# Kernel tuning notes

Measured on AMD Instinct MI355X. Metric: run time of the kernel, lower is better.

Reference implementation:

```python
import jax, jax.numpy as jnp
import numpy as np
import math

B, T, C = 4, 2048, 2048
N_HEAD, N_KV = 16, 4
HD = C // N_HEAD          # 128
N_REP = N_HEAD // N_KV    # 4


def setup_inputs() -> dict:
    key = jax.random.key(0)
    ks = jax.random.split(key, 5)
    x = jax.random.normal(ks[0], (B, T, C), dtype=jnp.float32)
    s = 0.02
    wq = jax.random.normal(ks[1], (C, N_HEAD * HD), dtype=jnp.float32) * s
    wk = jax.random.normal(ks[2], (C, N_KV * HD), dtype=jnp.float32) * s
    wv = jax.random.normal(ks[3], (C, N_KV * HD), dtype=jnp.float32) * s
    wo = jax.random.normal(ks[4], (C, C), dtype=jnp.float32) * s
    # RoPE table: cos/sin pairs, equivalent to torch polar freqs_cis (theta=10000)
    inv_freq = 1.0 / (10000.0 ** (jnp.arange(0, HD, 2, dtype=jnp.float32) / HD))  # (HD/2,)
    ang = jnp.arange(T, dtype=jnp.float32)[:, None] * inv_freq[None, :]           # (T, HD/2)
    freqs_cis = jnp.stack([jnp.cos(ang), jnp.sin(ang)], axis=-1)                  # (T, HD/2, 2)
    return {"x": x, "freqs_cis": freqs_cis, "wq": wq, "wk": wk, "wv": wv, "wo": wo}


def _rope(t, freqs_cis):
    # t: (B, T, H, HD); complex multiply on (even, odd) pairs
    tp = t.reshape(*t.shape[:-1], HD // 2, 2)
    a, b = tp[..., 0], tp[..., 1]
    c = freqs_cis[: t.shape[1], :, 0][None, :, None, :]  # (1,T,1,HD/2)
    s = freqs_cis[: t.shape[1], :, 1][None, :, None, :]
    out = jnp.stack([a * c - b * s, a * s + b * c], axis=-1)
    return out.reshape(t.shape).astype(t.dtype)


def reference(x, freqs_cis, wq, wk, wv, wo):
    q = (x @ wq).reshape(B, T, N_HEAD, HD)
    k = (x @ wk).reshape(B, T, N_KV, HD)
    v = (x @ wv).reshape(B, T, N_KV, HD)
    q = _rope(q, freqs_cis)
    k = _rope(k, freqs_cis)
    # GQA attention without materializing repeated K/V: group q heads by kv head
    qg = q.reshape(B, T, N_KV, N_REP, HD)
    scale = 1.0 / math.sqrt(HD)
    att = jnp.einsum('btgrd,bsgd->bgrts', qg, k) * scale   # (B,G,R,T,S)
    causal = jnp.tril(jnp.ones((T, T), dtype=bool))
    att = jnp.where(causal, att, jnp.finfo(att.dtype).min)
    att = jax.nn.softmax(att, axis=-1)
    y = jnp.einsum('bgrts,bsgd->btgrd', att, v).reshape(B, T, C)
    y = y @ wo
    return y
```

## Files before the change

### kernel.cpp

```cpp
#include <hip/hip_runtime.h>
#include <math.h>
#include <stdint.h>

#define B_ 4
#define T_ 2048
#define C_ 2048
#define NH 16
#define NKV 4
#define HD 128
#define NREP 4
#define KVC (NKV*HD)
#define QSTR 3072

typedef __attribute__((ext_vector_type(8))) __bf16 bf16x8;
typedef __attribute__((ext_vector_type(4))) float floatx4;

#define GLOBAL_AS __attribute__((address_space(1)))
#define LDS_AS __attribute__((address_space(3)))

__device__ __forceinline__ void gl2lds16(const unsigned short* g, unsigned short* l) {
  __builtin_amdgcn_global_load_lds((const GLOBAL_AS unsigned int*)g,
                                   (LDS_AS unsigned int*)l, 16, 0, 0);
}

__device__ __forceinline__ float b2f(unsigned short u) {
  union { unsigned int i; float f; } v; v.i = ((unsigned int)u) << 16; return v.f;
}
__device__ __forceinline__ unsigned short f2b(float f) {
  union { float f; unsigned int i; } v; v.f = f;
  unsigned int r = v.i + 0x7fffu + ((v.i >> 16) & 1u);
  return (unsigned short)(r >> 16);
}

__global__ void cvt_bf16_kernel(const float* __restrict__ X,
                                unsigned short* __restrict__ Y, int n) {
  int i = (blockIdx.x * 256 + threadIdx.x) * 4;
  if (i >= n) return;
  float4 v = *(const float4*)(X + i);
  ushort4 o;
  o.x = f2b(v.x); o.y = f2b(v.y); o.z = f2b(v.z); o.w = f2b(v.w);
  *(ushort4*)(Y + i) = o;
}

__global__ void transpose_cvt_kernel(const float* __restrict__ W,
                                     unsigned short* __restrict__ Wt,
                                     int K, int N) {
  __shared__ float tile[32][33];
  int n = blockIdx.x * 32 + threadIdx.x;
  int kbase = blockIdx.y * 32;
  #pragma unroll
  for (int i = 0; i < 32; i += 8)
    tile[threadIdx.y + i][threadIdx.x] = W[(size_t)(kbase + threadIdx.y + i) * N + n];
  __syncthreads();
  int k = kbase + threadIdx.x;
  int nb = blockIdx.x * 32;
  #pragma unroll
  for (int i = 0; i < 32; i += 8)
    Wt[(size_t)(nb + threadIdx.y + i) * K + k] = f2b(tile[threadIdx.x][threadIdx.y + i]);
}

__global__ void transpose_v_kernel(const unsigned short* __restrict__ V,
                                   unsigned short* __restrict__ Vt) {
  __shared__ unsigned short tile[32][33];
  int d0 = blockIdx.x * 32;
  int sg = blockIdx.y * 32;
  int b = sg >> 11;
  int s0 = sg & (T_ - 1);
  #pragma unroll
  for (int i = 0; i < 32; i += 8)
    tile[threadIdx.y + i][threadIdx.x] =
        V[(size_t)(sg + threadIdx.y + i) * QSTR + d0 + threadIdx.x];
  __syncthreads();
  #pragma unroll
  for (int i = 0; i < 32; i += 8) {
    int d = d0 + threadIdx.y + i;
    int g = d >> 7, dl = d & 127;
    Vt[((size_t)(b * NKV + g) * HD + dl) * T_ + s0 + threadIdx.x] =
        tile[threadIdx.x][threadIdx.y + i];
  }
}

template<int STORE_BF16>
__global__ __launch_bounds__(512, 2) void gemm256_bt(
    const unsigned short* __restrict__ A,
    const unsigned short* __restrict__ Bt,
    void* __restrict__ Cout,
    int M, int N, int K)
{
  __shared__ unsigned short Lds[65536];

  int tid = threadIdx.x;

  int nbx = gridDim.x;
  int nwg = nbx * gridDim.y;
  int orig = blockIdx.y * nbx + blockIdx.x;
  int cpx = nwg >> 3;
  int swz = (orig & 7) * cpx + (orig >> 3);
  int m0 = (swz % nbx) * 256;
  int n0 = (swz / nbx) * 256;

  int wave = tid >> 6, lane = tid & 63;
  int fr = lane & 15, kg = lane >> 4;
  int slot = kg ^ ((fr >> 1) & 3);
  int wm_off = (wave >> 2) * 128;
  int wn_off = (wave & 3) * 64;

  int rowoff = wave * 16 + (lane >> 2);
  int kgs = (lane & 3) ^ ((lane >> 3) & 3);
  const unsigned short* Asrc = A  + (size_t)(m0 + rowoff) * K + kgs * 8;
  const unsigned short* Bsrc = Bt + (size_t)(n0 + rowoff) * K + kgs * 8;
  size_t rstep = (size_t)128 * K;

  int abase = (wm_off + fr) * 32 + slot * 8;
  int bbase = 8192 + (wn_off + fr) * 32 + slot * 8;

  floatx4 acc[8][4];
  #pragma unroll
  for (int i = 0; i < 8; i++)
    #pragma unroll
    for (int j = 0; j < 4; j++)
      acc[i][j] = (floatx4){0.f, 0.f, 0.f, 0.f};

  int nt = K >> 6;

  #define STAGE_HALF(tn, kkh, isB) do {                                        \
    const unsigned short* s_ = ((isB) ? Bsrc : Asrc) + (size_t)(tn) * 64 + (kkh) * 32; \
    unsigned short* d_ = &Lds[(((tn) & 1) << 15) + ((kkh) << 14) + ((isB) << 13) + (wave << 9)]; \
    gl2lds16(s_, d_);                                                          \
    gl2lds16(s_ + rstep, d_ + 4096);                                           \
  } while (0)

  STAGE_HALF(0, 0, 0); STAGE_HALF(0, 0, 1); STAGE_HALF(0, 1, 0); STAGE_HALF(0, 1, 1);
  asm volatile("s_waitcnt vmcnt(4)" ::: "memory");
  __builtin_amdgcn_s_barrier();

  bf16x8 bfrag[4];
  for (int t = 0; t < nt; ++t) {
    int cb = (t & 1) << 15;
    int more = (t + 1 < nt);
    #pragma unroll
    for (int p = 0; p < 4; ++p) {
      const int kkc = p >> 1, mhc = p & 1;
      if (mhc == 0) {
        #pragma unroll
        for (int j = 0; j < 4; ++j) {
          union { uint4 u; bf16x8 v; } tb;
          tb.u = *(const uint4*)&Lds[cb + bbase + (kkc << 14) + j * 512];
          bfrag[j] = tb.v;
        }
      }
      bf16x8 af[4];
      #pragma unroll
      for (int i = 0; i < 4; ++i) {
        union { uint4 u; bf16x8 v; } ta;
        ta.u = *(const uint4*)&Lds[cb + abase + (kkc << 14) + (mhc * 4 + i) * 512];
        af[i] = ta.v;
      }
      if (more) STAGE_HALF(t + 1, kkc, mhc);
      if (p == 1) {
        if (more) asm volatile("s_waitcnt vmcnt(4)" ::: "memory");
        else      asm volatile("s_waitcnt vmcnt(0)" ::: "memory");
      } else if (p == 3) {
        if (more) asm volatile("s_waitcnt vmcnt(4)" ::: "memory");
      }
      __builtin_amdgcn_s_barrier();
      asm volatile("s_waitcnt lgkmcnt(0)" ::: "memory");
      __builtin_amdgcn_s_setprio(1);
      #pragma unroll
      for (int i = 0; i < 4; ++i)
        #pragma unroll
        for (int j = 0; j < 4; ++j)
          acc[mhc * 4 + i][j] =
              __builtin_amdgcn_mfma_f32_16x16x32_bf16(af[i], bfrag[j], acc[mhc * 4 + i][j], 0, 0, 0);
      __builtin_amdgcn_s_setprio(0);
      __builtin_amdgcn_s_barrier();
    }
  }
  #undef STAGE_HALF

  int erow = kg * 4;
  #pragma unroll
  for (int i = 0; i < 8; ++i)
    #pragma unroll
    for (int j = 0; j < 4; ++j) {
      int gm = m0 + wm_off + i * 16 + erow;
      int gn = n0 + wn_off + j * 16 + fr;
      #pragma unroll
      for (int r = 0; r < 4; ++r) {
        float v = acc[i][j][r];
        if (STORE_BF16)
          ((unsigned short*)Cout)[(size_t)(gm + r) * N + gn] = f2b(v);
        else
          ((float*)Cout)[(size_t)(gm + r) * N + gn] = v;
      }
    }
}

__global__ void rope_kernel(unsigned short* __restrict__ X,
                            const float* __restrict__ FC, int nheads, int stride) {
  long long idx = (long long)blockIdx.x * 256 + threadIdx.x;
  int p = (int)(idx & (HD / 2 - 1));
  long long t1 = idx >> 6;
  int h = (int)(t1 % nheads);
  long long row = t1 / nheads;
  int t = (int)(row & (T_ - 1));
  float c = FC[((size_t)t * (HD / 2) + p) * 2 + 0];
  float s = FC[((size_t)t * (HD / 2) + p) * 2 + 1];
  unsigned short* ptr = X + row * (size_t)stride + h * HD + 2 * p;
  float a = b2f(ptr[0]), b = b2f(ptr[1]);
  ptr[0] = f2b(a * c - b * s);
  ptr[1] = f2b(a * s + b * c);
}

#define ABR 128
#define ABC 64
#define KLD 136
#define VLD 72
#define PLD 72

__global__ __launch_bounds__(256, 3) void attn_mfma_kernel(
    const unsigned short* __restrict__ Q,
    const unsigned short* __restrict__ Kg,
    const unsigned short* __restrict__ Vt,
    unsigned short* __restrict__ O)
{
  __shared__ unsigned short KPs[128 * PLD];
  __shared__ unsigned short Vs[HD * VLD];

  int bh = blockIdx.x;
  int qt = (int)(gridDim.y - 1 - blockIdx.y);
  int b = bh >> 4, h = bh & 15, g = h >> 2;
  int tid = threadIdx.x, wave = tid >> 6, lane = tid & 63;
  int fr = lane & 15, kg = lane >> 4, erow = 4 * kg;

  bf16x8 qf[2][4];
  #pragma unroll
  for (int rt = 0; rt < 2; rt++) {
    const unsigned short* qrow =
        Q + (size_t)(b * T_ + qt * ABR + wave * 32 + rt * 16 + fr) * QSTR + h * HD;
    #pragma unroll
    for (int kk = 0; kk < 4; kk++) {
      union { uint4 u; bf16x8 v; } t;
      t.u = *(const uint4*)(qrow + kk * 32 + kg * 8);
      qf[rt][kk] = t.v;
    }
  }

  floatx4 oacc[2][8];
  #pragma unroll
  for (int rt = 0; rt < 2; rt++)
    #pragma unroll
    for (int d = 0; d < 8; d++) oacc[rt][d] = (floatx4){0.f, 0.f, 0.f, 0.f};
  float rsum[2][4];
  #pragma unroll
  for (int rt = 0; rt < 2; rt++)
    #pragma unroll
    for (int r = 0; r < 4; r++) rsum[rt][r] = 0.f;

  const float scale = 0.08838834764831845f;
  const float MOFF = 9.0f;

  size_t krow0 = (size_t)(b * T_) * QSTR + g * HD;
  size_t vbase = ((size_t)(b * NKV + g) * HD) * T_;
  int q0 = qt * ABR + wave * 32;
  int nit = 2 * qt + 2;

  int sr = tid >> 2, kc4 = (tid & 3) * 8;
  int vr = tid >> 1, vc = (tid & 1) * 8;

  for (int it = 0; it < nit; it++) {
    int s0 = it * ABC;
    __syncthreads();
    {
      const unsigned short* src = Kg + krow0 + (size_t)(s0 + sr) * QSTR;
      #pragma unroll
      for (int c = 0; c < 4; c++)
        *(uint4*)&KPs[sr * KLD + kc4 + c * 32] = *(const uint4*)(src + kc4 + c * 32);
      const unsigned short* vsrc = Vt + vbase + (size_t)vr * T_ + s0;
      #pragma unroll
      for (int c = 0; c < 4; c++)
        *(uint4*)&Vs[vr * VLD + vc + c * 16] = *(const uint4*)(vsrc + vc + c * 16);
    }
    __syncthreads();

    floatx4 scr[2][4];
    #pragma unroll
    for (int rt = 0; rt < 2; rt++)
      #pragma unroll
      for (int t = 0; t < 4; t++) scr[rt][t] = (floatx4){0.f, 0.f, 0.f, 0.f};
    __builtin_amdgcn_s_setprio(1);
    #pragma unroll
    for (int kk = 0; kk < 4; kk++) {
      #pragma unroll
      for (int t = 0; t < 4; t++) {
        union { uint4 u; bf16x8 v; } kf;
        kf.u = *(const uint4*)&KPs[(t * 16 + fr) * KLD + kk * 32 + kg * 8];
        scr[0][t] = __builtin_amdgcn_mfma_f32_16x16x32_bf16(qf[0][kk], kf.v, scr[0][t], 0, 0, 0);
        scr[1][t] = __builtin_amdgcn_mfma_f32_16x16x32_bf16(qf[1][kk], kf.v, scr[1][t], 0, 0, 0);
      }
    }
    __builtin_amdgcn_s_setprio(0);

    #pragma unroll
    for (int t = 0; t < 4; t++) {
      int s_g = s0 + t * 16 + fr;
      #pragma unroll
      for (int rt = 0; rt < 2; rt++)
        #pragma unroll
        for (int r = 0; r < 4; r++) {
          int qrow = q0 + rt * 16 + erow + r;
          float p = (s_g <= qrow) ? __expf(scr[rt][t][r] * scale - MOFF) : 0.f;
          scr[rt][t][r] = p;
          rsum[rt][r] += p;
        }
    }
    __syncthreads();

    #pragma unroll
    for (int rt = 0; rt < 2; rt++)
      #pragma unroll
      for (int t = 0; t < 4; t++)
        #pragma unroll
        for (int r = 0; r < 4; r++)
          KPs[(wave * 32 + rt * 16 + erow + r) * PLD + t * 16 + fr] = f2b(scr[rt][t][r]);

    bf16x8 pf[2][2];
    #pragma unroll
    for (int rt = 0; rt < 2; rt++)
      #pragma unroll
      for (int kk = 0; kk < 2; kk++) {
        union { uint4 u; bf16x8 v; } t;
        t.u = *(const uint4*)&KPs[(wave * 32 + rt * 16 + fr) * PLD + kk * 32 + kg * 8];
        pf[rt][kk] = t.v;
      }
    __builtin_amdgcn_s_setprio(1);
    #pragma unroll
    for (int d = 0; d < 8; d++)
      #pragma unroll
      for (int kk = 0; kk < 2; kk++) {
        union { uint4 u; bf16x8 v; } vf;
        vf.u = *(const uint4*)&Vs[(d * 16 + fr) * VLD + kk * 32 + kg * 8];
        oacc[0][d] = __builtin_amdgcn_mfma_f32_16x16x32_bf16(pf[0][kk], vf.v, oacc[0][d], 0, 0, 0);
        oacc[1][d] = __builtin_amdgcn_mfma_f32_16x16x32_bf16(pf[1][kk], vf.v, oacc[1][d], 0, 0, 0);
      }
    __builtin_amdgcn_s_setprio(0);
  }

  #pragma unroll
  for (int rt = 0; rt < 2; rt++)
    #pragma unroll
    for (int r = 0; r < 4; r++) {
      float s = rsum[rt][r];
      s += __shfl_xor(s, 1); s += __shfl_xor(s, 2);
      s += __shfl_xor(s, 4); s += __shfl_xor(s, 8);
      rsum[rt][r] = s;
    }

  #pragma unroll
  for (int rt = 0; rt < 2; rt++)
    #pragma unroll
    for (int r = 0; r < 4; r++) {
      float inv = 1.f / rsum[rt][r];
      size_t orow =
          (size_t)(b * T_ + qt * ABR + wave * 32 + rt * 16 + erow + r) * C_ + h * HD;
      #pragma unroll
      for (int d = 0; d < 8; d++)
        O[orow + d * 16 + fr] = f2b(oacc[rt][d][r] * inv);
    }
}

extern "C" void kernel_launch(void* const* d_in, const int* in_sizes, int n_in,
                              void* d_out, int out_size, void* d_ws, size_t ws_size,
                              hipStream_t stream) {
  (void)in_sizes; (void)n_in; (void)out_size; (void)ws_size;
  const float* x  = (const float*)d_in[0];
  const float* fc = (const float*)d_in[1];
  const float* wq = (const float*)d_in[2];
  const float* wk = (const float*)d_in[3];
  const float* wv = (const float*)d_in[4];
  const float* wo = (const float*)d_in[5];
  float* out = (float*)d_out;

  char* ws = (char*)d_ws;
  unsigned short* xb   = (unsigned short*)(ws);
  unsigned short* qkv  = (unsigned short*)(ws + 33554432);
  unsigned short* wqT  = (unsigned short*)(ws + 83886080);
  unsigned short* wkT  = (unsigned short*)(ws + 92274688);
  unsigned short* wvT  = (unsigned short*)(ws + 94371840);
  unsigned short* woT  = (unsigned short*)(ws + 96468992);
  unsigned short* vt   = wqT;
  unsigned short* yb   = xb;

  int nx = B_ * T_ * C_;
  cvt_bf16_kernel<<<nx / 4 / 256, 256, 0, stream>>>(x, xb, nx);
  transpose_cvt_kernel<<<dim3(C_ / 32, C_ / 32), dim3(32, 8), 0, stream>>>(wq, wqT, C_, C_);
  transpose_cvt_kernel<<<dim3(KVC / 32, C_ / 32), dim3(32, 8), 0, stream>>>(wk, wkT, C_, KVC);
  transpose_cvt_kernel<<<dim3(KVC / 32, C_ / 32), dim3(32, 8), 0, stream>>>(wv, wvT, C_, KVC);
  transpose_cvt_kernel<<<dim3(C_ / 32, C_ / 32), dim3(32, 8), 0, stream>>>(wo, woT, C_, C_);

  int M = B_ * T_;
  gemm256_bt<1><<<dim3(M / 256, QSTR / 256), 512, 0, stream>>>(xb, wqT, qkv, M, QSTR, C_);

  long long qp = (long long)B_ * T_ * NH * (HD / 2);
  rope_kernel<<<(unsigned)(qp / 256), 256, 0, stream>>>(qkv, fc, NH, QSTR);
  long long kp = (long long)B_ * T_ * NKV * (HD / 2);
  rope_kernel<<<(unsigned)(kp / 256), 256, 0, stream>>>(qkv + 2048, fc, NKV, QSTR);

  transpose_v_kernel<<<dim3(KVC / 32, B_ * T_ / 32), dim3(32, 8), 0, stream>>>(qkv + 2560, vt);

  attn_mfma_kernel<<<dim3(B_ * NH, T_ / ABR), 256, 0, stream>>>(qkv, qkv + 2048, vt, yb);

  gemm256_bt<0><<<dim3(M / 256, C_ / 256), 512, 0, stream>>>(yb, woT, out, M, C_, C_);
}
```

Baseline: 532.4 us.

## Prefetch K/V tiles into registers and transpose score MFMA for vectorized P stores

Global loads for the next K/V tile are issued into registers before the PV MFMA loop, so their latency overlaps with compute; the loop top then only copies registers into LDS. The QK MFMA operands are swapped so each lane holds four consecutive key positions for one query row. This allows P to be written to LDS as one bf16x4 store instead of four scalar stores, and reduces per-row sums to two shuffles. The cost is extra registers for the prefetch buffers, which may lower occupancy.

```diff
diff --git a/kernel.cpp b/kernel.cpp
--- a/kernel.cpp
+++ b/kernel.cpp
@@ -13,6 +13,7 @@
 #define QSTR 3072
 
 typedef __attribute__((ext_vector_type(8))) __bf16 bf16x8;
+typedef __attribute__((ext_vector_type(4))) __bf16 bf16x4;
 typedef __attribute__((ext_vector_type(4))) float floatx4;
 
 #define GLOBAL_AS __attribute__((address_space(1)))
@@ -251,11 +252,8 @@
   for (int rt = 0; rt < 2; rt++)
     #pragma unroll
     for (int d = 0; d < 8; d++) oacc[rt][d] = (floatx4){0.f, 0.f, 0.f, 0.f};
-  float rsum[2][4];
-  #pragma unroll
-  for (int rt = 0; rt < 2; rt++)
-    #pragma unroll
-    for (int r = 0; r < 4; r++) rsum[rt][r] = 0.f;
+  float rsum[2];
+  rsum[0] = 0.f; rsum[1] = 0.f;
 
   const float scale = 0.08838834764831845f;
   const float MOFF = 9.0f;
@@ -268,19 +266,23 @@
   int sr = tid >> 2, kc4 = (tid & 3) * 8;
   int vr = tid >> 1, vc = (tid & 1) * 8;
 
+  const unsigned short* kptr = Kg + krow0 + (size_t)sr * QSTR + kc4;
+  const unsigned short* vptr = Vt + vbase + (size_t)vr * T_ + vc;
+  uint4 gk[4], gv[4];
+  #pragma unroll
+  for (int c = 0; c < 4; c++) gk[c] = *(const uint4*)(kptr + c * 32);
+  #pragma unroll
+  for (int c = 0; c < 4; c++) gv[c] = *(const uint4*)(vptr + c * 16);
+
   for (int it = 0; it < nit; it++) {
     int s0 = it * ABC;
     __syncthreads();
-    {
-      const unsigned short* src = Kg + krow0 + (size_t)(s0 + sr) * QSTR;
-      #pragma unroll
-      for (int c = 0; c < 4; c++)
-        *(uint4*)&KPs[sr * KLD + kc4 + c * 32] = *(const uint4*)(src + kc4 + c * 32);
-      const unsigned short* vsrc = Vt + vbase + (size_t)vr * T_ + s0;
-      #pragma unroll
-      for (int c = 0; c < 4; c++)
-        *(uint4*)&Vs[vr * VLD + vc + c * 16] = *(const uint4*)(vsrc + vc + c * 16);
-    }
+    #pragma unroll
+    for (int c = 0; c < 4; c++)
+      *(uint4*)&KPs[sr * KLD + kc4 + c * 32] = gk[c];
+    #pragma unroll
+    for (int c = 0; c < 4; c++)
+      *(uint4*)&Vs[vr * VLD + vc + c * 16] = gv[c];
     __syncthreads();
 
     floatx4 scr[2][4];
@@ -295,23 +297,23 @@
       for (int t = 0; t < 4; t++) {
         union { uint4 u; bf16x8 v; } kf;
         kf.u = *(const uint4*)&KPs[(t * 16 + fr) * KLD + kk * 32 + kg * 8];
-        scr[0][t] = __builtin_amdgcn_mfma_f32_16x16x32_bf16(qf[0][kk], kf.v, scr[0][t], 0, 0, 0);
-        scr[1][t] = __builtin_amdgcn_mfma_f32_16x16x32_bf16(qf[1][kk], kf.v, scr[1][t], 0, 0, 0);
+        scr[0][t] = __builtin_amdgcn_mfma_f32_16x16x32_bf16(kf.v, qf[0][kk], scr[0][t], 0, 0, 0);
+        scr[1][t] = __builtin_amdgcn_mfma_f32_16x16x32_bf16(kf.v, qf[1][kk], scr[1][t], 0, 0, 0);
       }
     }
     __builtin_amdgcn_s_setprio(0);
 
     #pragma unroll
-    for (int t = 0; t < 4; t++) {
-      int s_g = s0 + t * 16 + fr;
-      #pragma unroll
-      for (int rt = 0; rt < 2; rt++)
+    for (int rt = 0; rt < 2; rt++) {
+      int qrow = q0 + rt * 16 + fr;
+      #pragma unroll
+      for (int t = 0; t < 4; t++)
         #pragma unroll
         for (int r = 0; r < 4; r++) {
-          int qrow = q0 + rt * 16 + erow + r;
+          int s_g = s0 + t * 16 + erow + r;
           float p = (s_g <= qrow) ? __expf(scr[rt][t][r] * scale - MOFF) : 0.f;
           scr[rt][t][r] = p;
-          rsum[rt][r] += p;
+          rsum[rt] += p;
         }
     }
     __syncthreads();
@@ -319,10 +321,14 @@
     #pragma unroll
     for (int rt = 0; rt < 2; rt++)
       #pragma unroll
-      for (int t = 0; t < 4; t++)
-        #pragma unroll
-        for (int r = 0; r < 4; r++)
-          KPs[(wave * 32 + rt * 16 + erow + r) * PLD + t * 16 + fr] = f2b(scr[rt][t][r]);
+      for (int t = 0; t < 4; t++) {
+        bf16x4 pw;
+        pw[0] = (__bf16)scr[rt][t][0];
+        pw[1] = (__bf16)scr[rt][t][1];
+        pw[2] = (__bf16)scr[rt][t][2];
+        pw[3] = (__bf16)scr[rt][t][3];
+        *(bf16x4*)&KPs[(wave * 32 + rt * 16 + fr) * PLD + t * 16 + erow] = pw;
+      }
 
     bf16x8 pf[2][2];
     #pragma unroll
@@ -333,6 +339,16 @@
         t.u = *(const uint4*)&KPs[(wave * 32 + rt * 16 + fr) * PLD + kk * 32 + kg * 8];
         pf[rt][kk] = t.v;
       }
+
+    if (it + 1 < nit) {
+      kptr += (size_t)ABC * QSTR;
+      vptr += ABC;
+      #pragma unroll
+      for (int c = 0; c < 4; c++) gk[c] = *(const uint4*)(kptr + c * 32);
+      #pragma unroll
+      for (int c = 0; c < 4; c++) gv[c] = *(const uint4*)(vptr + c * 16);
+    }
+
     __builtin_amdgcn_s_setprio(1);
     #pragma unroll
     for (int d = 0; d < 8; d++)
@@ -347,20 +363,18 @@
   }
 
   #pragma unroll
+  for (int rt = 0; rt < 2; rt++) {
+    float s = rsum[rt];
+    s += __shfl_xor(s, 16);
+    s += __shfl_xor(s, 32);
+    rsum[rt] = s;
+  }
+
+  #pragma unroll
   for (int rt = 0; rt < 2; rt++)
     #pragma unroll
     for (int r = 0; r < 4; r++) {
-      float s = rsum[rt][r];
-      s += __shfl_xor(s, 1); s += __shfl_xor(s, 2);
-      s += __shfl_xor(s, 4); s += __shfl_xor(s, 8);
-      rsum[rt][r] = s;
-    }
-
-  #pragma unroll
-  for (int rt = 0; rt < 2; rt++)
-    #pragma unroll
-    for (int r = 0; r < 4; r++) {
-      float inv = 1.f / rsum[rt][r];
+      float inv = 1.f / __shfl(rsum[rt], erow + r);
       size_t orow =
           (size_t)(b * T_ + qt * ABR + wave * 32 + rt * 16 + erow + r) * C_ + h * HD;
       #pragma unroll
```

Result: slower. 598.9 us (+12.5%).
